# Optimization experiments

Hardware: AMD Instinct MI355X
Metric: run time of the kernel (lower is better)

Reference implementation:

```python
import jax, jax.numpy as jnp
import numpy as np

HEADS = 16
NEG_INF = -1e30


def rel_shift(t):
    # t: [b, h, i, j] with i == j; Transformer-XL style relative shift
    b, h, i, j = t.shape
    t = jnp.pad(t, ((0, 0), (0, 0), (0, 0), (1, 0)))  # zero pad on last dim front
    t = t.reshape(b, h, j + 1, i)[:, :, 1:]
    return t.reshape(b, h, i, j)


def setup_inputs() -> dict:
    key = jax.random.key(0)
    ks = jax.random.split(key, 8)
    b, n, dim = 2, 2048, 1024
    d_head = dim // HEADS
    w = 0.02
    return {
        "x": jax.random.normal(ks[0], (b, n, dim), dtype=jnp.float32),
        "pos_emb": jax.random.normal(ks[1], (n, dim), dtype=jnp.float32),
        "Wq": jax.random.normal(ks[2], (dim, dim), dtype=jnp.float32) * w,
        "bq": jnp.zeros((dim,), dtype=jnp.float32),
        "Wkv": jax.random.normal(ks[3], (dim, 2 * dim), dtype=jnp.float32) * w,
        "bkv": jnp.zeros((2 * dim,), dtype=jnp.float32),
        "Wp": jax.random.normal(ks[4], (dim, d_head), dtype=jnp.float32) * w,
        "bp": jnp.zeros((d_head,), dtype=jnp.float32),
        "Wo": jax.random.normal(ks[5], (dim, dim), dtype=jnp.float32) * w,
        "bo": jnp.zeros((dim,), dtype=jnp.float32),
    }


def reference(x, pos_emb, Wq, bq, Wkv, bkv, Wp, bp, Wo, bo):
    b, n, dim = x.shape
    h = HEADS
    d = dim // h
    scale = d ** -0.5

    q = (x @ Wq + bq).reshape(b, n, h, d).transpose(0, 2, 1, 3)  # b h n d
    kv = x @ Wkv + bkv
    k, v = jnp.split(kv, 2, axis=-1)
    k = k.reshape(b, n, h, d).transpose(0, 2, 1, 3)
    v = v.reshape(b, n, h, d).transpose(0, 2, 1, 3)

    dots = jnp.einsum('bhid,bhjd->bhij', q, k) * scale

    # relative position bias
    p = pos_emb @ Wp + bp  # [n, d]
    pos_attn = jnp.einsum('bhid,jd->bhij', q, p) * scale
    dots = dots + rel_shift(pos_attn)

    # causal mask
    causal = jnp.triu(jnp.ones((n, n), dtype=bool), 1)
    dots = jnp.where(causal[None, None], NEG_INF, dots)

    attn = jax.nn.softmax(dots, axis=-1)
    out = jnp.einsum('bhij,bhjd->bhid', attn, v)
    out = out.transpose(0, 2, 1, 3).reshape(b, n, dim)
    return out @ Wo + bo
```

## Files before the change

### kernel.cpp

```cpp
#include <hip/hip_runtime.h>
#include <hip/hip_bf16.h>
#include <cstdint>
#include <cstddef>

#define SEQ_N 2048
#define DIM   1024
#define NHEAD 16
#define DH    64

typedef __bf16 bf16;
typedef __attribute__((ext_vector_type(8))) __bf16 bf16x8;
typedef __attribute__((ext_vector_type(4))) __bf16 bf16x4;
typedef __attribute__((ext_vector_type(4))) float f32x4;

__device__ __forceinline__ void gl_lds16(const bf16* g, bf16* l) {
    __builtin_amdgcn_global_load_lds(
        (const __attribute__((address_space(1))) unsigned int*)g,
        (__attribute__((address_space(3))) unsigned int*)l, 16, 0, 0);
}

__global__ __launch_bounds__(256) void prep_kernel(
    const float* __restrict__ x, const float* __restrict__ pos,
    const float* __restrict__ Wq, const float* __restrict__ Wkv,
    const float* __restrict__ Wo, const float* __restrict__ Wp,
    bf16* __restrict__ xb, bf16* __restrict__ posb,
    bf16* __restrict__ WqkvT, bf16* __restrict__ WoT, bf16* __restrict__ WpT)
{
    int bid = blockIdx.x;
    if (bid < 6144) {
        const int NX = 4096 * 1024;
        int i = (bid * 256 + threadIdx.x) * 4;
        if (i < NX) {
            float4 v = *(const float4*)&x[i];
            xb[i + 0] = (bf16)v.x; xb[i + 1] = (bf16)v.y;
            xb[i + 2] = (bf16)v.z; xb[i + 3] = (bf16)v.w;
        } else {
            int j = i - NX;
            float4 v = *(const float4*)&pos[j];
            posb[j + 0] = (bf16)v.x; posb[j + 1] = (bf16)v.y;
            posb[j + 2] = (bf16)v.z; posb[j + 3] = (bf16)v.w;
        }
        return;
    }
    __shared__ float t[32][33];
    bid -= 6144;
    const float* src; bf16* dst; int tidx, nx, N;
    if (bid < 1024)      { src = Wq;  dst = WqkvT;                       tidx = bid;        nx = 32; N = 1024; }
    else if (bid < 3072) { src = Wkv; dst = WqkvT + (size_t)1024 * 1024; tidx = bid - 1024; nx = 64; N = 2048; }
    else if (bid < 4096) { src = Wo;  dst = WoT;                         tidx = bid - 3072; nx = 32; N = 1024; }
    else                 { src = Wp;  dst = WpT;                         tidx = bid - 4096; nx = 2;  N = 64;   }
    int n0 = (tidx % nx) * 32, k0 = (tidx / nx) * 32;
    int tx = threadIdx.x & 31, ty = threadIdx.x >> 5;
    #pragma unroll
    for (int r = ty; r < 32; r += 8)
        t[r][tx] = src[(size_t)(k0 + r) * N + n0 + tx];
    __syncthreads();
    #pragma unroll
    for (int r = ty; r < 32; r += 8)
        dst[(size_t)(n0 + r) * 1024 + k0 + tx] = (bf16)t[tx][r];
}

__global__ __launch_bounds__(256) void qkvp_kernel(
    const bf16* __restrict__ xb, const bf16* __restrict__ WqkvT,
    const bf16* __restrict__ posb, const bf16* __restrict__ WpT,
    const float* __restrict__ bq, const float* __restrict__ bkv,
    const float* __restrict__ bp,
    bf16* __restrict__ qbuf, bf16* __restrict__ kbuf,
    bf16* __restrict__ vtbuf, bf16* __restrict__ pfrag)
{
    __shared__ __align__(16) bf16 sm[128 * 132];
    bf16* At = sm;
    bf16* Bt = sm + 128 * 64;
    const int tid = threadIdx.x, w = tid >> 6, lane = tid & 63;
    const int q = lane >> 4, ln15 = lane & 15;
    const int lr = lane >> 3, c_log = (lane & 7) ^ lr;
    const int bx = blockIdx.x, by = blockIdx.y;
    const int m0 = by * 128;

    if (bx == 24) {
        if (by >= 16) return;
        f32x4 acc[2][4] = {};
        for (int k0 = 0; k0 < 1024; k0 += 64) {
            __syncthreads();
            #pragma unroll
            for (int t = 0; t < 4; ++t)
                gl_lds16(&posb[(size_t)(m0 + 32 * w + 8 * t + lr) * 1024 + k0 + c_log * 8],
                         &At[(32 * w + 8 * t) * 64]);
            #pragma unroll
            for (int t = 0; t < 2; ++t)
                gl_lds16(&WpT[(size_t)(16 * w + 8 * t + lr) * 1024 + k0 + c_log * 8],
                         &Bt[(16 * w + 8 * t) * 64]);
            __syncthreads();
            bf16x8 bfr[2][4];
            #pragma unroll
            for (int ks = 0; ks < 2; ++ks)
                #pragma unroll
                for (int sn = 0; sn < 4; ++sn) {
                    int rb = 16 * sn + ln15;
                    bfr[ks][sn] = *(const bf16x8*)&Bt[(rb * 8 + ((4 * ks + q) ^ (rb & 7))) * 8];
                }
            #pragma unroll
            for (int sm2 = 0; sm2 < 2; ++sm2) {
                int ra = 32 * w + 16 * sm2 + ln15;
                #pragma unroll
                for (int ks = 0; ks < 2; ++ks) {
                    bf16x8 af = *(const bf16x8*)&At[(ra * 8 + ((4 * ks + q) ^ (ra & 7))) * 8];
                    #pragma unroll
                    for (int sn = 0; sn < 4; ++sn)
                        acc[sm2][sn] = __builtin_amdgcn_mfma_f32_16x16x32_bf16(
                            af, bfr[ks][sn], acc[sm2][sn], 0, 0, 0);
                }
            }
        }
        #pragma unroll
        for (int sm2 = 0; sm2 < 2; ++sm2)
            #pragma unroll
            for (int sn = 0; sn < 4; ++sn)
                #pragma unroll
                for (int r = 0; r < 4; ++r) {
                    int row = m0 + 32 * w + 16 * sm2 + 4 * q + r;
                    int d = 16 * sn + ln15;
                    int sb = row >> 4, lnp = row & 15;
                    int ks2 = d >> 5, qd = (d >> 3) & 3, e = d & 7;
                    pfrag[(((size_t)sb * 2 + ks2) * 64 + qd * 16 + lnp) * 8 + e] =
                        (bf16)(acc[sm2][sn][r] + bp[d]);
                }
        return;
    }

    const int n0 = bx * 128;
    const int wm = w >> 1, wn = w & 1;
    f32x4 acc[4][4] = {};

    for (int k0 = 0; k0 < 1024; k0 += 64) {
        __syncthreads();
        #pragma unroll
        for (int t = 0; t < 4; ++t) {
            int r = 32 * w + 8 * t + lr;
            gl_lds16(&xb[(size_t)(m0 + r) * 1024 + k0 + c_log * 8],
                     &At[(32 * w + 8 * t) * 64]);
            gl_lds16(&WqkvT[(size_t)(n0 + r) * 1024 + k0 + c_log * 8],
                     &Bt[(32 * w + 8 * t) * 64]);
        }
        __syncthreads();

        bf16x8 af[2][4], bfr[2][4];
        #pragma unroll
        for (int ks = 0; ks < 2; ++ks)
            #pragma unroll
            for (int s = 0; s < 4; ++s) {
                int ra = 64 * wm + 16 * s + ln15;
                af[ks][s]  = *(const bf16x8*)&At[(ra * 8 + ((4 * ks + q) ^ (ra & 7))) * 8];
                int rb = 64 * wn + 16 * s + ln15;
                bfr[ks][s] = *(const bf16x8*)&Bt[(rb * 8 + ((4 * ks + q) ^ (rb & 7))) * 8];
            }
        #pragma unroll
        for (int ks = 0; ks < 2; ++ks)
            #pragma unroll
            for (int si = 0; si < 4; ++si)
                #pragma unroll
                for (int sj = 0; sj < 4; ++sj)
                    acc[si][sj] = __builtin_amdgcn_mfma_f32_16x16x32_bf16(
                        af[ks][si], bfr[ks][sj], acc[si][sj], 0, 0, 0);
    }

    if (bx < 16) {
        #pragma unroll
        for (int si = 0; si < 4; ++si)
            #pragma unroll
            for (int sj = 0; sj < 4; ++sj)
                #pragma unroll
                for (int r = 0; r < 4; ++r) {
                    int row = m0 + 64 * wm + 16 * si + 4 * q + r;
                    int col = n0 + 64 * wn + 16 * sj + ln15;
                    float v = acc[si][sj][r] + (col < 1024 ? bq[col] : bkv[col - 1024]);
                    if (col < 1024) qbuf[(size_t)row * 1024 + col] = (bf16)v;
                    else            kbuf[(size_t)row * 1024 + (col - 1024)] = (bf16)v;
                }
    } else {
        __syncthreads();
        #pragma unroll
        for (int si = 0; si < 4; ++si)
            #pragma unroll
            for (int sj = 0; sj < 4; ++sj) {
                int dL = 64 * wn + 16 * sj + ln15;
                int tL = 64 * wm + 16 * si + 4 * q;
                float bias = bkv[1024 + (bx - 16) * 128 + dL];
                bf16x4 o4;
                #pragma unroll
                for (int r = 0; r < 4; ++r)
                    o4[r] = (bf16)(acc[si][sj][r] + bias);
                *(bf16x4*)&sm[dL * 132 + tL] = o4;
            }
        __syncthreads();
        const int b = m0 >> 11;
        const int t0 = m0 & 2047;
        const int h0 = (bx - 16) * 2;
        #pragma unroll
        for (int p = 0; p < 16; ++p) {
            int d = (tid >> 5) + 8 * p;
            int t = (tid & 31) * 4;
            bf16x4 v4 = *(const bf16x4*)&sm[d * 132 + t];
            int rowv = (b * NHEAD + h0 + (d >> 6)) * DH + (d & 63);
            *(bf16x4*)&vtbuf[(size_t)rowv * SEQ_N + t0 + t] = v4;
        }
    }
}

__global__ __launch_bounds__(256, 4) void attn_mfma_kernel(
    const bf16* __restrict__ qb,
    const bf16* __restrict__ kb,
    const bf16* __restrict__ vt,
    const bf16* __restrict__ pfrag,
    bf16* __restrict__ ob)
{
    const int bh = blockIdx.y, bi = bh >> 4, hh = bh & 15;
    const int qblk = ((blockIdx.y >> 3) & 1) ? (31 - (int)blockIdx.x)
                                             : (int)blockIdx.x;
    const int i0 = qblk << 6;
    const int tid = threadIdx.x, w = tid >> 6, lane = tid & 63;
    const int q = lane >> 4, ln15 = lane & 15;
    const int lr = lane >> 3, c_log = (lane & 7) ^ lr;

    __shared__ __align__(16) bf16 smem[17664];
    bf16* Qs  = smem;
    bf16* S2L = smem + w * 1344;
    bf16* Ks  = smem + 5376;
    bf16* Vs  = smem + 9472;
    bf16* Pw  = smem + 13568 + w * 1024;

    const bf16* qbase = qb + ((size_t)(bi * SEQ_N + i0)) * DIM + hh * DH;
    const bf16* kbase = kb + ((size_t)bi * SEQ_N) * DIM + hh * DH;
    const bf16* vbase = vt + ((size_t)(bi * NHEAD + hh) * DH) * SEQ_N;

    #pragma unroll
    for (int t = 0; t < 2; ++t)
        gl_lds16(qbase + (size_t)(16 * w + 8 * t + lr) * DIM + c_log * 8,
                 &Qs[(16 * w + 8 * t) * 64]);
    __syncthreads();
    bf16x8 qf0, qf1;
    {
        int rq = 16 * w + ln15;
        qf0 = *(const bf16x8*)&Qs[(rq * 8 + ((q    ) ^ (rq & 7))) * 8];
        qf1 = *(const bf16x8*)&Qs[(rq * 8 + ((4 + q) ^ (rq & 7))) * 8];
    }
    __syncthreads();

    const int A0 = 127 - 4 * qblk - w;
    f32x4 s2r4;
    {
        bf16x8 f0 = *(const bf16x8*)&pfrag[(((size_t)A0 * 2 + 0) * 64 + lane) * 8];
        bf16x8 f1 = *(const bf16x8*)&pfrag[(((size_t)A0 * 2 + 1) * 64 + lane) * 8];
        f32x4 a = {0.f, 0.f, 0.f, 0.f};
        a = __builtin_amdgcn_mfma_f32_16x16x32_bf16(f0, qf0, a, 0, 0, 0);
        a = __builtin_amdgcn_mfma_f32_16x16x32_bf16(f1, qf1, a, 0, 0, 0);
        s2r4 = a;
    }

    float m_run = -1e30f, l_run = 0.f;
    f32x4 O_T[4] = {};

    for (int jt = 0; jt <= qblk; ++jt) {
        const int j0 = jt << 6;

        bf16x8 pfA[4][2];
        #pragma unroll
        for (int s = 1; s <= 4; ++s) {
            int sb = A0 + 4 * jt + s;
            if (sb > 127) sb = 127;
            pfA[s-1][0] = *(const bf16x8*)&pfrag[(((size_t)sb * 2 + 0) * 64 + lane) * 8];
            pfA[s-1][1] = *(const bf16x8*)&pfrag[(((size_t)sb * 2 + 1) * 64 + lane) * 8];
        }
        #pragma unroll
        for (int t = 0; t < 2; ++t) {
            int r = 16 * w + 8 * t + lr;
            gl_lds16(kbase + (size_t)(j0 + r) * DIM + c_log * 8,
                     &Ks[(16 * w + 8 * t) * 64]);
            gl_lds16(vbase + (size_t)r * SEQ_N + j0 + c_log * 8,
                     &Vs[(16 * w + 8 * t) * 64]);
        }

        f32x4 s2r[5];
        s2r[0] = s2r4;
        #pragma unroll
        for (int s = 1; s <= 4; ++s) {
            f32x4 a = {0.f, 0.f, 0.f, 0.f};
            a = __builtin_amdgcn_mfma_f32_16x16x32_bf16(pfA[s-1][0], qf0, a, 0, 0, 0);
            a = __builtin_amdgcn_mfma_f32_16x16x32_bf16(pfA[s-1][1], qf1, a, 0, 0, 0);
            s2r[s] = a;
        }
        s2r4 = s2r[4];
        #pragma unroll
        for (int s = 0; s < 5; ++s)
            #pragma unroll
            for (int r = 0; r < 4; ++r)
                S2L[ln15 * 84 + 16 * s + 4 * q + r] = (bf16)s2r[s][r];

        __syncthreads();

        float sv[4][4];
        #pragma unroll
        for (int sn = 0; sn < 4; ++sn) {
            int rk = 16 * sn + ln15;
            bf16x8 k0f = *(const bf16x8*)&Ks[(rk * 8 + ((q    ) ^ (rk & 7))) * 8];
            bf16x8 k1f = *(const bf16x8*)&Ks[(rk * 8 + ((4 + q) ^ (rk & 7))) * 8];
            f32x4 a = {0.f, 0.f, 0.f, 0.f};
            a = __builtin_amdgcn_mfma_f32_16x16x32_bf16(k0f, qf0, a, 0, 0, 0);
            a = __builtin_amdgcn_mfma_f32_16x16x32_bf16(k1f, qf1, a, 0, 0, 0);
            #pragma unroll
            for (int r = 0; r < 4; ++r) {
                int jl = 16 * sn + 4 * q + r;
                float b = (float)S2L[ln15 * 84 + 15 - ln15 + jl];
                sv[sn][r] = (a[r] + b) * 0.125f;
            }
        }
        if (jt == qblk) {
            #pragma unroll
            for (int sn = 0; sn < 4; ++sn)
                #pragma unroll
                for (int r = 0; r < 4; ++r)
                    if (16 * sn + 4 * q + r > 16 * w + ln15)
                        sv[sn][r] = -1e30f;
        }

        float mx = sv[0][0];
        #pragma unroll
        for (int sn = 0; sn < 4; ++sn)
            #pragma unroll
            for (int r = 0; r < 4; ++r)
                mx = fmaxf(mx, sv[sn][r]);
        mx = fmaxf(mx, __shfl_xor(mx, 16));
        mx = fmaxf(mx, __shfl_xor(mx, 32));
        const float mn = fmaxf(m_run, mx);
        float sum = 0.f;
        #pragma unroll
        for (int sn = 0; sn < 4; ++sn)
            #pragma unroll
            for (int r = 0; r < 4; ++r) {
                float e = __expf(sv[sn][r] - mn);
                sv[sn][r] = e;
                sum += e;
            }
        sum += __shfl_xor(sum, 16);
        sum += __shfl_xor(sum, 32);
        const float alpha = __expf(m_run - mn);
        l_run = l_run * alpha + sum;
        m_run = mn;

        #pragma unroll
        for (int sn = 0; sn < 4; ++sn)
            #pragma unroll
            for (int r = 0; r < 4; ++r) {
                int chunk = (2 * sn + (q >> 1)) ^ (ln15 & 7);
                Pw[ln15 * 64 + chunk * 8 + 4 * (q & 1) + r] = (bf16)sv[sn][r];
            }
        #pragma unroll
        for (int sd = 0; sd < 4; ++sd)
            #pragma unroll
            for (int r = 0; r < 4; ++r)
                O_T[sd][r] *= alpha;

        __builtin_amdgcn_s_waitcnt(0);

        #pragma unroll
        for (int ks = 0; ks < 2; ++ks) {
            bf16x8 pT = *(const bf16x8*)&Pw[ln15 * 64 + (((4 * ks + q) ^ (ln15 & 7))) * 8];
            #pragma unroll
            for (int sd = 0; sd < 4; ++sd) {
                int rv = 16 * sd + ln15;
                bf16x8 vf = *(const bf16x8*)&Vs[(rv * 8 + ((4 * ks + q) ^ (rv & 7))) * 8];
                O_T[sd] = __builtin_amdgcn_mfma_f32_16x16x32_bf16(vf, pT, O_T[sd], 0, 0, 0);
            }
        }
        __syncthreads();
    }

    const float inv = 1.0f / l_run;
    const size_t row = (size_t)bi * SEQ_N + i0 + 16 * w + ln15;
    #pragma unroll
    for (int sd = 0; sd < 4; ++sd) {
        bf16x4 o4;
        #pragma unroll
        for (int r = 0; r < 4; ++r)
            o4[r] = (bf16)(O_T[sd][r] * inv);
        *(bf16x4*)&ob[row * DIM + hh * DH + 16 * sd + 4 * q] = o4;
    }
}

__global__ __launch_bounds__(256) void outproj_kernel(
    const bf16* __restrict__ ab, const bf16* __restrict__ WoT,
    const float* __restrict__ bo, float* __restrict__ out)
{
    __shared__ __align__(16) bf16 At[128 * 64];
    __shared__ __align__(16) bf16 Bt[64 * 64];
    const int tid = threadIdx.x, w = tid >> 6, lane = tid & 63;
    const int q = lane >> 4, ln15 = lane & 15;
    const int lr = lane >> 3, c_log = (lane & 7) ^ lr;
    const int m0 = blockIdx.y * 128, n0 = blockIdx.x * 64;

    f32x4 acc[2][4] = {};
    for (int k0 = 0; k0 < 1024; k0 += 64) {
        __syncthreads();
        #pragma unroll
        for (int t = 0; t < 4; ++t)
            gl_lds16(&ab[(size_t)(m0 + 32 * w + 8 * t + lr) * 1024 + k0 + c_log * 8],
                     &At[(32 * w + 8 * t) * 64]);
        #pragma unroll
        for (int t = 0; t < 2; ++t)
            gl_lds16(&WoT[(size_t)(n0 + 16 * w + 8 * t + lr) * 1024 + k0 + c_log * 8],
                     &Bt[(16 * w + 8 * t) * 64]);
        __syncthreads();

        bf16x8 bfr[2][4];
        #pragma unroll
        for (int ks = 0; ks < 2; ++ks)
            #pragma unroll
            for (int sn = 0; sn < 4; ++sn) {
                int rb = 16 * sn + ln15;
                bfr[ks][sn] = *(const bf16x8*)&Bt[(rb * 8 + ((4 * ks + q) ^ (rb & 7))) * 8];
            }
        #pragma unroll
        for (int sm2 = 0; sm2 < 2; ++sm2) {
            int ra = 32 * w + 16 * sm2 + ln15;
            #pragma unroll
            for (int ks = 0; ks < 2; ++ks) {
                bf16x8 af = *(const bf16x8*)&At[(ra * 8 + ((4 * ks + q) ^ (ra & 7))) * 8];
                #pragma unroll
                for (int sn = 0; sn < 4; ++sn)
                    acc[sm2][sn] = __builtin_amdgcn_mfma_f32_16x16x32_bf16(
                        af, bfr[ks][sn], acc[sm2][sn], 0, 0, 0);
            }
        }
    }
    #pragma unroll
    for (int sm2 = 0; sm2 < 2; ++sm2)
        #pragma unroll
        for (int sn = 0; sn < 4; ++sn) {
            int col = n0 + 16 * sn + ln15;
            float bias = bo[col];
            #pragma unroll
            for (int r = 0; r < 4; ++r) {
                int row = m0 + 32 * w + 16 * sm2 + 4 * q + r;
                out[(size_t)row * 1024 + col] = acc[sm2][sn][r] + bias;
            }
        }
}

extern "C" void kernel_launch(void* const* d_in, const int* in_sizes, int n_in,
                              void* d_out, int out_size, void* d_ws, size_t ws_size,
                              hipStream_t stream)
{
    const float* x    = (const float*)d_in[0];
    const float* pos  = (const float*)d_in[1];
    const float* Wq   = (const float*)d_in[2];
    const float* bq   = (const float*)d_in[3];
    const float* Wkv  = (const float*)d_in[4];
    const float* bkv  = (const float*)d_in[5];
    const float* Wp   = (const float*)d_in[6];
    const float* bp   = (const float*)d_in[7];
    const float* Wo   = (const float*)d_in[8];
    const float* bo   = (const float*)d_in[9];
    float* out = (float*)d_out;

    const int M = 2 * SEQ_N;
    char* ws = (char*)d_ws;
    bf16* xb     = (bf16*)ws;  ws += (size_t)M * DIM * 2;
    bf16* posb   = (bf16*)ws;  ws += (size_t)SEQ_N * DIM * 2;
    bf16* WqkvT  = (bf16*)ws;  ws += (size_t)3072 * 1024 * 2;
    bf16* WoT    = (bf16*)ws;  ws += (size_t)DIM * DIM * 2;
    bf16* WpT    = (bf16*)ws;  ws += (size_t)DH * DIM * 2;
    bf16* qbuf   = (bf16*)ws;  ws += (size_t)M * DIM * 2;
    bf16* kbuf   = (bf16*)ws;  ws += (size_t)M * DIM * 2;
    bf16* vtbuf  = (bf16*)ws;  ws += (size_t)M * DIM * 2;
    bf16* pfrag  = (bf16*)ws;  ws += (size_t)512 * 1024;
    bf16* abuf   = (bf16*)ws;

    dim3 blk(256);
    prep_kernel<<<dim3(10304), blk, 0, stream>>>(
        x, pos, Wq, Wkv, Wo, Wp, xb, posb, WqkvT, WoT, WpT);

    qkvp_kernel<<<dim3(25, 32), blk, 0, stream>>>(
        xb, WqkvT, posb, WpT, bq, bkv, bp, qbuf, kbuf, vtbuf, pfrag);

    attn_mfma_kernel<<<dim3(32, 32), blk, 0, stream>>>(
        qbuf, kbuf, vtbuf, pfrag, abuf);

    outproj_kernel<<<dim3(16, 32), blk, 0, stream>>>(
        abuf, WoT, bo, out);
}
```

Before: 249.0 us.

## Split long causal query blocks across two KV halves and merge with a separate kernel

The attention grid becomes a flat 1536-block launch. Query blocks 16–31 are split into two KV-range halves whose partial O, max and sum go to workspace scratch, and a new merge kernel combines them with log-sum-exp weights. Blocks are ordered so each XCD handles a fixed group of heads. The softmax scale and log2(e) are folded into Q at projection time so exp2f can be used, and the positional bias now seeds the MFMA accumulator. The output rescale is skipped when the running max does not change, s_setprio wraps the MFMA sections, and Q fragments are read straight from global memory instead of staged through LDS. The aim is to balance the causal triangle's uneven work and trim per-tile ALU cost, at the price of an extra kernel launch and a round trip of partial results through memory that reuses the input workspace region.

```diff
diff --git a/kernel.cpp b/kernel.cpp
--- a/kernel.cpp
+++ b/kernel.cpp
@@ -165,6 +165,7 @@
     }
 
     if (bx < 16) {
+        const float QSCL = 0.125f * 1.44269504088896341f;
         #pragma unroll
         for (int si = 0; si < 4; ++si)
             #pragma unroll
@@ -174,7 +175,7 @@
                     int row = m0 + 64 * wm + 16 * si + 4 * q + r;
                     int col = n0 + 64 * wn + 16 * sj + ln15;
                     float v = acc[si][sj][r] + (col < 1024 ? bq[col] : bkv[col - 1024]);
-                    if (col < 1024) qbuf[(size_t)row * 1024 + col] = (bf16)v;
+                    if (col < 1024) qbuf[(size_t)row * 1024 + col] = (bf16)(v * QSCL);
                     else            kbuf[(size_t)row * 1024 + (col - 1024)] = (bf16)v;
                 }
     } else {
@@ -212,18 +213,29 @@
     const bf16* __restrict__ kb,
     const bf16* __restrict__ vt,
     const bf16* __restrict__ pfrag,
-    bf16* __restrict__ ob)
+    bf16* __restrict__ ob,
+    float* __restrict__ Opart,
+    float2* __restrict__ MLpart)
 {
-    const int bh = blockIdx.y, bi = bh >> 4, hh = bh & 15;
-    const int qblk = ((blockIdx.y >> 3) & 1) ? (31 - (int)blockIdx.x)
-                                             : (int)blockIdx.x;
+    const int f   = (int)blockIdx.x;
+    const int xcd = f & 7;
+    const int jj  = f >> 3;
+    const int s   = jj >> 2;
+    const int bh  = xcd * 4 + (jj & 3);
+    int qblk, lo, hi, part;
+    if (s < 16) { qblk = 16 + s; lo = 0; hi = 16; part = 0; }
+    else {
+        int k = (s - 16) >> 1;
+        if (((s - 16) & 1) == 0) { qblk = 31 - k; lo = 16; hi = qblk + 1; part = 1; }
+        else                     { qblk = 15 - k; lo = 0;  hi = qblk + 1; part = -1; }
+    }
+    const int bi = bh >> 4, hh = bh & 15;
     const int i0 = qblk << 6;
     const int tid = threadIdx.x, w = tid >> 6, lane = tid & 63;
     const int q = lane >> 4, ln15 = lane & 15;
     const int lr = lane >> 3, c_log = (lane & 7) ^ lr;
 
     __shared__ __align__(16) bf16 smem[17664];
-    bf16* Qs  = smem;
     bf16* S2L = smem + w * 1344;
     bf16* Ks  = smem + 5376;
     bf16* Vs  = smem + 9472;
@@ -233,24 +245,15 @@
     const bf16* kbase = kb + ((size_t)bi * SEQ_N) * DIM + hh * DH;
     const bf16* vbase = vt + ((size_t)(bi * NHEAD + hh) * DH) * SEQ_N;
 
-    #pragma unroll
-    for (int t = 0; t < 2; ++t)
-        gl_lds16(qbase + (size_t)(16 * w + 8 * t + lr) * DIM + c_log * 8,
-                 &Qs[(16 * w + 8 * t) * 64]);
-    __syncthreads();
-    bf16x8 qf0, qf1;
-    {
-        int rq = 16 * w + ln15;
-        qf0 = *(const bf16x8*)&Qs[(rq * 8 + ((q    ) ^ (rq & 7))) * 8];
-        qf1 = *(const bf16x8*)&Qs[(rq * 8 + ((4 + q) ^ (rq & 7))) * 8];
-    }
-    __syncthreads();
+    bf16x8 qf0 = *(const bf16x8*)&qbase[(size_t)(16 * w + ln15) * DIM + q * 8];
+    bf16x8 qf1 = *(const bf16x8*)&qbase[(size_t)(16 * w + ln15) * DIM + 32 + q * 8];
 
     const int A0 = 127 - 4 * qblk - w;
     f32x4 s2r4;
     {
-        bf16x8 f0 = *(const bf16x8*)&pfrag[(((size_t)A0 * 2 + 0) * 64 + lane) * 8];
-        bf16x8 f1 = *(const bf16x8*)&pfrag[(((size_t)A0 * 2 + 1) * 64 + lane) * 8];
+        int sb0 = A0 + 4 * lo;
+        bf16x8 f0 = *(const bf16x8*)&pfrag[(((size_t)sb0 * 2 + 0) * 64 + lane) * 8];
+        bf16x8 f1 = *(const bf16x8*)&pfrag[(((size_t)sb0 * 2 + 1) * 64 + lane) * 8];
         f32x4 a = {0.f, 0.f, 0.f, 0.f};
         a = __builtin_amdgcn_mfma_f32_16x16x32_bf16(f0, qf0, a, 0, 0, 0);
         a = __builtin_amdgcn_mfma_f32_16x16x32_bf16(f1, qf1, a, 0, 0, 0);
@@ -260,16 +263,16 @@
     float m_run = -1e30f, l_run = 0.f;
     f32x4 O_T[4] = {};
 
-    for (int jt = 0; jt <= qblk; ++jt) {
+    for (int jt = lo; jt < hi; ++jt) {
         const int j0 = jt << 6;
 
         bf16x8 pfA[4][2];
         #pragma unroll
-        for (int s = 1; s <= 4; ++s) {
-            int sb = A0 + 4 * jt + s;
+        for (int ss = 1; ss <= 4; ++ss) {
+            int sb = A0 + 4 * jt + ss;
             if (sb > 127) sb = 127;
-            pfA[s-1][0] = *(const bf16x8*)&pfrag[(((size_t)sb * 2 + 0) * 64 + lane) * 8];
-            pfA[s-1][1] = *(const bf16x8*)&pfrag[(((size_t)sb * 2 + 1) * 64 + lane) * 8];
+            pfA[ss-1][0] = *(const bf16x8*)&pfrag[(((size_t)sb * 2 + 0) * 64 + lane) * 8];
+            pfA[ss-1][1] = *(const bf16x8*)&pfrag[(((size_t)sb * 2 + 1) * 64 + lane) * 8];
         }
         #pragma unroll
         for (int t = 0; t < 2; ++t) {
@@ -280,40 +283,44 @@
                      &Vs[(16 * w + 8 * t) * 64]);
         }
 
-        f32x4 s2r[5];
-        s2r[0] = s2r4;
-        #pragma unroll
-        for (int s = 1; s <= 4; ++s) {
-            f32x4 a = {0.f, 0.f, 0.f, 0.f};
-            a = __builtin_amdgcn_mfma_f32_16x16x32_bf16(pfA[s-1][0], qf0, a, 0, 0, 0);
-            a = __builtin_amdgcn_mfma_f32_16x16x32_bf16(pfA[s-1][1], qf1, a, 0, 0, 0);
-            s2r[s] = a;
-        }
-        s2r4 = s2r[4];
-        #pragma unroll
-        for (int s = 0; s < 5; ++s)
-            #pragma unroll
-            for (int r = 0; r < 4; ++r)
-                S2L[ln15 * 84 + 16 * s + 4 * q + r] = (bf16)s2r[s][r];
+        {
+            f32x4 s2r[5];
+            s2r[0] = s2r4;
+            #pragma unroll
+            for (int ss = 1; ss <= 4; ++ss) {
+                f32x4 a = {0.f, 0.f, 0.f, 0.f};
+                a = __builtin_amdgcn_mfma_f32_16x16x32_bf16(pfA[ss-1][0], qf0, a, 0, 0, 0);
+                a = __builtin_amdgcn_mfma_f32_16x16x32_bf16(pfA[ss-1][1], qf1, a, 0, 0, 0);
+                s2r[ss] = a;
+            }
+            s2r4 = s2r[4];
+            #pragma unroll
+            for (int ss = 0; ss < 5; ++ss)
+                #pragma unroll
+                for (int r = 0; r < 4; ++r)
+                    S2L[ln15 * 84 + 16 * ss + 4 * q + r] = (bf16)s2r[ss][r];
+        }
 
         __syncthreads();
 
         float sv[4][4];
+        __builtin_amdgcn_s_setprio(1);
         #pragma unroll
         for (int sn = 0; sn < 4; ++sn) {
             int rk = 16 * sn + ln15;
             bf16x8 k0f = *(const bf16x8*)&Ks[(rk * 8 + ((q    ) ^ (rk & 7))) * 8];
             bf16x8 k1f = *(const bf16x8*)&Ks[(rk * 8 + ((4 + q) ^ (rk & 7))) * 8];
-            f32x4 a = {0.f, 0.f, 0.f, 0.f};
+            f32x4 a;
+            #pragma unroll
+            for (int r = 0; r < 4; ++r)
+                a[r] = (float)S2L[ln15 * 84 + 15 - ln15 + 16 * sn + 4 * q + r];
             a = __builtin_amdgcn_mfma_f32_16x16x32_bf16(k0f, qf0, a, 0, 0, 0);
             a = __builtin_amdgcn_mfma_f32_16x16x32_bf16(k1f, qf1, a, 0, 0, 0);
             #pragma unroll
-            for (int r = 0; r < 4; ++r) {
-                int jl = 16 * sn + 4 * q + r;
-                float b = (float)S2L[ln15 * 84 + 15 - ln15 + jl];
-                sv[sn][r] = (a[r] + b) * 0.125f;
-            }
-        }
+            for (int r = 0; r < 4; ++r)
+                sv[sn][r] = a[r];
+        }
+        __builtin_amdgcn_s_setprio(0);
         if (jt == qblk) {
             #pragma unroll
             for (int sn = 0; sn < 4; ++sn)
@@ -337,14 +344,23 @@
         for (int sn = 0; sn < 4; ++sn)
             #pragma unroll
             for (int r = 0; r < 4; ++r) {
-                float e = __expf(sv[sn][r] - mn);
+                float e = exp2f(sv[sn][r] - mn);
                 sv[sn][r] = e;
                 sum += e;
             }
         sum += __shfl_xor(sum, 16);
         sum += __shfl_xor(sum, 32);
-        const float alpha = __expf(m_run - mn);
-        l_run = l_run * alpha + sum;
+        if (__all(mx <= m_run)) {
+            l_run += sum;
+        } else {
+            const float alpha = exp2f(m_run - mn);
+            l_run = l_run * alpha + sum;
+            #pragma unroll
+            for (int sd = 0; sd < 4; ++sd)
+                #pragma unroll
+                for (int r = 0; r < 4; ++r)
+                    O_T[sd][r] *= alpha;
+        }
         m_run = mn;
 
         #pragma unroll
@@ -354,14 +370,10 @@
                 int chunk = (2 * sn + (q >> 1)) ^ (ln15 & 7);
                 Pw[ln15 * 64 + chunk * 8 + 4 * (q & 1) + r] = (bf16)sv[sn][r];
             }
-        #pragma unroll
-        for (int sd = 0; sd < 4; ++sd)
-            #pragma unroll
-            for (int r = 0; r < 4; ++r)
-                O_T[sd][r] *= alpha;
 
         __builtin_amdgcn_s_waitcnt(0);
 
+        __builtin_amdgcn_s_setprio(1);
         #pragma unroll
         for (int ks = 0; ks < 2; ++ks) {
             bf16x8 pT = *(const bf16x8*)&Pw[ln15 * 64 + (((4 * ks + q) ^ (ln15 & 7))) * 8];
@@ -372,18 +384,62 @@
                 O_T[sd] = __builtin_amdgcn_mfma_f32_16x16x32_bf16(vf, pT, O_T[sd], 0, 0, 0);
             }
         }
-        __syncthreads();
-    }
-
-    const float inv = 1.0f / l_run;
-    const size_t row = (size_t)bi * SEQ_N + i0 + 16 * w + ln15;
+        __builtin_amdgcn_s_setprio(0);
+        __syncthreads();
+    }
+
+    const int row = 16 * w + ln15;
+    if (part < 0) {
+        const float inv = 1.0f / l_run;
+        const size_t grow = (size_t)bi * SEQ_N + i0 + row;
+        #pragma unroll
+        for (int sd = 0; sd < 4; ++sd) {
+            bf16x4 o4;
+            #pragma unroll
+            for (int r = 0; r < 4; ++r)
+                o4[r] = (bf16)(O_T[sd][r] * inv);
+            *(bf16x4*)&ob[grow * DIM + hh * DH + 16 * sd + 4 * q] = o4;
+        }
+    } else {
+        const int slot = (bh * 16 + (qblk - 16)) * 2 + part;
+        float* op = Opart + (size_t)slot * 4096 + row * 64;
+        #pragma unroll
+        for (int sd = 0; sd < 4; ++sd)
+            *(f32x4*)&op[16 * sd + 4 * q] = O_T[sd];
+        if (lane < 16)
+            MLpart[slot * 64 + row] = make_float2(m_run, l_run);
+    }
+}
+
+__global__ __launch_bounds__(256) void merge_kernel(
+    const float* __restrict__ Opart, const float2* __restrict__ MLpart,
+    bf16* __restrict__ ob)
+{
+    const int pb = blockIdx.x;
+    const int bh = pb >> 4, qblk = 16 + (pb & 15);
+    const int bi = bh >> 4, hh = bh & 15;
+    const int row = threadIdx.x >> 2;
+    const int d0 = (threadIdx.x & 3) * 16;
+
+    float2 ml0 = MLpart[(pb * 2 + 0) * 64 + row];
+    float2 ml1 = MLpart[(pb * 2 + 1) * 64 + row];
+    float m = fmaxf(ml0.x, ml1.x);
+    float a0 = exp2f(ml0.x - m), a1 = exp2f(ml1.x - m);
+    float inv = 1.0f / (ml0.y * a0 + ml1.y * a1);
+
+    const float* o0 = Opart + ((size_t)(pb * 2 + 0)) * 4096 + row * 64 + d0;
+    const float* o1 = Opart + ((size_t)(pb * 2 + 1)) * 4096 + row * 64 + d0;
+    bf16* dst = ob + ((size_t)(bi * SEQ_N + qblk * 64 + row)) * DIM + hh * DH + d0;
     #pragma unroll
-    for (int sd = 0; sd < 4; ++sd) {
+    for (int k = 0; k < 4; ++k) {
+        float4 v0 = *(const float4*)&o0[4 * k];
+        float4 v1 = *(const float4*)&o1[4 * k];
         bf16x4 o4;
-        #pragma unroll
-        for (int r = 0; r < 4; ++r)
-            o4[r] = (bf16)(O_T[sd][r] * inv);
-        *(bf16x4*)&ob[row * DIM + hh * DH + 16 * sd + 4 * q] = o4;
+        o4[0] = (bf16)((v0.x * a0 + v1.x * a1) * inv);
+        o4[1] = (bf16)((v0.y * a0 + v1.y * a1) * inv);
+        o4[2] = (bf16)((v0.z * a0 + v1.z * a1) * inv);
+        o4[3] = (bf16)((v0.w * a0 + v1.w * a1) * inv);
+        *(bf16x4*)&dst[4 * k] = o4;
     }
 }
 
@@ -475,6 +531,9 @@
     bf16* pfrag  = (bf16*)ws;  ws += (size_t)512 * 1024;
     bf16* abuf   = (bf16*)ws;
 
+    float*  Opart  = (float*)d_ws;
+    float2* MLpart = (float2*)((char*)d_ws + (size_t)1024 * 4096 * 4);
+
     dim3 blk(256);
     prep_kernel<<<dim3(10304), blk, 0, stream>>>(
         x, pos, Wq, Wkv, Wo, Wp, xb, posb, WqkvT, WoT, WpT);
@@ -482,8 +541,10 @@
     qkvp_kernel<<<dim3(25, 32), blk, 0, stream>>>(
         xb, WqkvT, posb, WpT, bq, bkv, bp, qbuf, kbuf, vtbuf, pfrag);
 
-    attn_mfma_kernel<<<dim3(32, 32), blk, 0, stream>>>(
-        qbuf, kbuf, vtbuf, pfrag, abuf);
+    attn_mfma_kernel<<<dim3(1536), blk, 0, stream>>>(
+        qbuf, kbuf, vtbuf, pfrag, abuf, Opart, MLpart);
+
+    merge_kernel<<<dim3(512), blk, 0, stream>>>(Opart, MLpart, abuf);
 
     outproj_kernel<<<dim3(16, 32), blk, 0, stream>>>(
         abuf, WoT, bo, out);
```

Measured after the change: 244.9 us. No clear change (-1.6%).
